# Kernel optimization log

Hardware: AMD Instinct MI355X
Metric: run time of the kernel (lower is better)

Reference implementation:

```python
import jax, jax.numpy as jnp
import numpy as np
import math

B, S, HID = 8, 512, 1024
H, D = 16, 64
SI = 64
MAXP = 512


def setup_inputs() -> dict:
    key = jax.random.key(0)
    ks = jax.random.split(key, 8)
    s = 1.0 / math.sqrt(HID)
    return {
        "hidden_states": jax.random.normal(ks[0], (B, S, HID), jnp.float32),
        "instruct_hidden_states": jax.random.normal(ks[1], (B, SI, HID), jnp.float32),
        "attention_mask": jnp.zeros((B, 1, 1, S), jnp.float32),
        "instruct_attention_mask": jnp.zeros((B, 1, 1, SI), jnp.float32),
        "Wq": jax.random.normal(ks[2], (HID, HID), jnp.float32) * s,
        "bq": jnp.zeros((HID,), jnp.float32),
        "Wk": jax.random.normal(ks[3], (HID, HID), jnp.float32) * s,
        "bk": jnp.zeros((HID,), jnp.float32),
        "Wv": jax.random.normal(ks[4], (HID, HID), jnp.float32) * s,
        "bv": jnp.zeros((HID,), jnp.float32),
        "dist_emb": jax.random.normal(ks[5], (2 * MAXP - 1, D), jnp.float32) * 0.02,
        "gate": jax.random.normal(ks[6], (1, H, 1, 1), jnp.float32) * 0.1,
    }


def _heads(x):
    # [B, L, H*D] -> [B, H, L, D]
    b, l, _ = x.shape
    return x.reshape(b, l, H, D).transpose(0, 2, 1, 3)


def reference(hidden_states, instruct_hidden_states, attention_mask,
              instruct_attention_mask, Wq, bq, Wk, bk, Wv, bv, dist_emb, gate):
    scale = 1.0 / math.sqrt(D)
    q = _heads(hidden_states @ Wq + bq)               # [B,H,S,D]
    k = _heads(hidden_states @ Wk + bk)
    v = _heads(hidden_states @ Wv + bv)
    ik = _heads(instruct_hidden_states @ Wk + bk)     # [B,H,Si,D]
    iv = _heads(instruct_hidden_states @ Wv + bv)

    # self-attention scores with relative_key_query position bias
    scores = jnp.einsum('bhld,bhrd->bhlr', q, k)
    pos = jnp.arange(S)
    dist = pos[:, None] - pos[None, :] + (MAXP - 1)   # [S,S] in [0, 2*MAXP-2]
    pe = dist_emb[dist]                                # [S,S,D]
    scores = scores + jnp.einsum('bhld,lrd->bhlr', q, pe) \
                    + jnp.einsum('bhrd,lrd->bhlr', k, pe)
    scores = scores * scale + attention_mask
    probs = jax.nn.softmax(scores, axis=-1)
    ctx = jnp.einsum('bhlr,bhrd->bhld', probs, v)

    # gated instruct attention branch
    iscores = jnp.einsum('bhld,bhrd->bhlr', q, ik) * scale + instruct_attention_mask
    iprobs = jax.nn.softmax(iscores, axis=-1)
    ictx = jnp.einsum('bhlr,bhrd->bhld', iprobs, iv)
    ctx = ctx + jnp.tanh(gate) * ictx

    return ctx.transpose(0, 2, 1, 3).reshape(B, S, HID)
```

## Files before the change

kernel.cpp:

```cpp
#include <hip/hip_runtime.h>

#define NH 16
#define DH 64
#define SEQ 512
#define SIN 64
#define NBATCH 8

#define L2E 1.4426950408889634f
#define C2  0.18033688011112043f
#define DEFER_THR 11.5412435f

typedef short bf16x8 __attribute__((ext_vector_type(8)));
typedef short bf16x4 __attribute__((ext_vector_type(4)));
typedef float f32x4 __attribute__((ext_vector_type(4)));

__device__ __forceinline__ unsigned short f2bf(float f) {
  union { float f; unsigned u; } v; v.f = f;
  unsigned r = v.u + 0x7FFFu + ((v.u >> 16) & 1u);
  return (unsigned short)(r >> 16);
}
__device__ __forceinline__ float bf2f(unsigned short b) {
  union { unsigned u; float f; } v; v.u = ((unsigned)b) << 16;
  return v.f;
}
__device__ __forceinline__ f32x4 mfma16(bf16x8 a, bf16x8 b, f32x4 c) {
  return __builtin_amdgcn_mfma_f32_16x16x32_bf16(a, b, c, 0, 0, 0);
}
__device__ __forceinline__ void gload_lds16(const unsigned short* g, unsigned short* l) {
  __builtin_amdgcn_global_load_lds((const __attribute__((address_space(1))) void*)g,
                                   (__attribute__((address_space(3))) void*)l, 16, 0, 0);
}

__device__ __forceinline__ void stage_tile_swz(const unsigned short* g, int gstride,
                                               unsigned short* lds, int w, int lane) {
  #pragma unroll
  for (int c = 0; c < 2; ++c) {
    const int row = w * 16 + c * 8 + (lane >> 3);
    const int cb = ((lane & 7) ^ (lane >> 3)) << 4;
    gload_lds16(g + (size_t)row * gstride + (cb >> 1),
                lds + (w * 16 + c * 8) * 64);
  }
}
__device__ __forceinline__ bf16x8 read_swz(const unsigned short* lds, int row, int colbyte) {
  return *(const bf16x8*)((const char*)(lds + row * 64) + (colbyte ^ ((row & 7) << 4)));
}

__global__ __launch_bounds__(256) void k_convert_all(const float* __restrict__ hs,
                                                     const float* __restrict__ ihs,
                                                     const float* __restrict__ de,
                                                     const float* __restrict__ Wq,
                                                     const float* __restrict__ Wk,
                                                     const float* __restrict__ Wv,
                                                     unsigned short* __restrict__ X,
                                                     unsigned short* __restrict__ E,
                                                     unsigned short* __restrict__ Wt) {
  __shared__ float t[64][65];
  const int bx = blockIdx.x, tid = threadIdx.x;
  if (bx < 4608) {
    int idx = bx * 256 + tid;
    float4 v;
    if (idx < 1048576) v = ((const float4*)hs)[idx];
    else               v = ((const float4*)ihs)[idx - 1048576];
    ushort4 o; o.x = f2bf(v.x); o.y = f2bf(v.y); o.z = f2bf(v.z); o.w = f2bf(v.w);
    ((ushort4*)X)[idx] = o;
  } else if (bx < 5376) {
    const int wb = bx - 4608;
    const int z = wb >> 8, rem = wb & 255;
    const float* W = (z == 0) ? Wq : (z == 1) ? Wk : Wv;
    const int n0 = (rem & 15) * 64, k0 = (rem >> 4) * 64;
    #pragma unroll
    for (int q = 0; q < 4; ++q) {
      int s = q * 256 + tid;
      int r = s >> 4, c4 = s & 15;
      float4 v = *(const float4*)(W + (size_t)(k0 + r) * 1024 + n0 + c4 * 4);
      t[r][c4 * 4 + 0] = v.x; t[r][c4 * 4 + 1] = v.y;
      t[r][c4 * 4 + 2] = v.z; t[r][c4 * 4 + 3] = v.w;
    }
    __syncthreads();
    #pragma unroll
    for (int q = 0; q < 4; ++q) {
      int s = q * 256 + tid;
      int rn = s >> 4, c4 = s & 15;
      ushort4 o;
      o.x = f2bf(t[c4 * 4 + 0][rn]); o.y = f2bf(t[c4 * 4 + 1][rn]);
      o.z = f2bf(t[c4 * 4 + 2][rn]); o.w = f2bf(t[c4 * 4 + 3][rn]);
      *(ushort4*)(Wt + ((size_t)(z << 10) + n0 + rn) * 1024 + k0 + c4 * 4) = o;
    }
  } else {
    int idx = (bx - 5376) * 256 + tid;
    ushort4 o;
    if (idx < 16368) {
      float4 v = ((const float4*)de)[idx];
      o.x = f2bf(v.x); o.y = f2bf(v.y); o.z = f2bf(v.z); o.w = f2bf(v.w);
    } else { o.x = 0; o.y = 0; o.z = 0; o.w = 0; }
    ((ushort4*)E)[idx] = o;
  }
}

__global__ __launch_bounds__(256) void k_gemm(const unsigned short* __restrict__ X,
                                              const unsigned short* __restrict__ Wt,
                                              const float* __restrict__ bq,
                                              const float* __restrict__ bk,
                                              const float* __restrict__ bv,
                                              unsigned short* __restrict__ Q,
                                              unsigned short* __restrict__ K,
                                              unsigned short* __restrict__ Vt,
                                              unsigned short* __restrict__ IK,
                                              unsigned short* __restrict__ IVt) {
  __shared__ unsigned short smem[16384];
  const int tid = threadIdx.x, lane = tid & 63, w = tid >> 6;
  const int lg = lane >> 4, lc = lane & 15;
  const int m0 = blockIdx.y * 128, n0 = blockIdx.x * 128;
  const int wm = (w >> 1) * 64, wn = (w & 1) * 64;
  const int which = n0 >> 10;
  const int h0 = (n0 & 1023) >> 6;
  const float* barr = (which == 0) ? bq : (which == 1) ? bk : bv;

  f32x4 acc[4][4];
  #pragma unroll
  for (int i = 0; i < 4; ++i)
    #pragma unroll
    for (int j = 0; j < 4; ++j) acc[i][j] = (f32x4){0.f, 0.f, 0.f, 0.f};

  const int ca = w * 128 + lane, cb2 = ca + 64;
  const unsigned short* ap0 = X  + (size_t)(m0 + (ca  >> 2)) * 1024 + (ca  & 3) * 8;
  const unsigned short* ap1 = X  + (size_t)(m0 + (cb2 >> 2)) * 1024 + (cb2 & 3) * 8;
  const unsigned short* bp0 = Wt + (size_t)(n0 + (ca  >> 2)) * 1024 + (ca  & 3) * 8;
  const unsigned short* bp1 = Wt + (size_t)(n0 + (cb2 >> 2)) * 1024 + (cb2 & 3) * 8;

  #define STAGE(bi)                                                   \
    {                                                                 \
      gload_lds16(ap0, smem + (bi) * 4096 + (w * 128) * 8);           \
      gload_lds16(ap1, smem + (bi) * 4096 + (w * 128 + 64) * 8);      \
      gload_lds16(bp0, smem + 8192 + (bi) * 4096 + (w * 128) * 8);    \
      gload_lds16(bp1, smem + 8192 + (bi) * 4096 + (w * 128 + 64) * 8); \
      ap0 += 32; ap1 += 32; bp0 += 32; bp1 += 32;                     \
    }

  STAGE(0);
  int cur = 0;
  for (int kt = 0; kt < 32; ++kt) {
    __syncthreads();
    if (kt + 1 < 32) STAGE(cur ^ 1);
    const unsigned short* A = smem + cur * 4096;
    const unsigned short* B = smem + 8192 + cur * 4096;
    bf16x8 af[4], bfr[4];
    #pragma unroll
    for (int i = 0; i < 4; ++i)
      af[i] = *(const bf16x8*)(A + (wm + i * 16 + lc) * 32 + lg * 8);
    #pragma unroll
    for (int j = 0; j < 4; ++j)
      bfr[j] = *(const bf16x8*)(B + (wn + j * 16 + lc) * 32 + lg * 8);
    #pragma unroll
    for (int i = 0; i < 4; ++i)
      #pragma unroll
      for (int j = 0; j < 4; ++j)
        acc[i][j] = mfma16(af[i], bfr[j], acc[i][j]);
    cur ^= 1;
  }
  #undef STAGE

  __syncthreads();
  {
    char* Cs = (char*)smem;
    #pragma unroll
    for (int j = 0; j < 4; ++j) {
      const float bias = barr[(n0 & 1023) + wn + j * 16 + lc];
      #pragma unroll
      for (int i = 0; i < 4; ++i)
        #pragma unroll
        for (int ii = 0; ii < 4; ++ii) {
          int row = wm + i * 16 + lg * 4 + ii;
          int col = wn + j * 16 + lc;
          if (which == 2) { int t = row; row = col; col = t; }
          *(unsigned short*)(Cs + row * 256 + ((col * 2) ^ ((row & 7) << 4))) =
              f2bf(acc[i][j][ii] + bias);
        }
    }
  }
  __syncthreads();
  {
    const char* Cs = (const char*)smem;
    const int row = tid >> 1, half = tid & 1;
    uint4 cvec[8];
    #pragma unroll
    for (int c8 = 0; c8 < 8; ++c8) {
      const int colb = half * 128 + c8 * 16;
      cvec[c8] = *(const uint4*)(Cs + row * 256 + (colb ^ ((row & 7) << 4)));
    }
    unsigned short* dst = nullptr;
    if (which != 2) {
      const int gm = m0 + row, hh = h0 + half;
      if (gm < 4096) {
        const int bb = gm >> 9, ss = gm & 511;
        unsigned short* base = (which == 0) ? Q : K;
        dst = base + (((size_t)(bb * NH + hh) * 512 + ss) << 6);
      } else if (which == 1) {
        const int mi = gm - 4096, bb = mi >> 6, si = mi & 63;
        dst = IK + (((size_t)(bb * NH + hh) * 64 + si) << 6);
      }
    } else {
      const int dd = row, hh = h0 + (dd >> 6), ddl = dd & 63;
      if (m0 < 4096) {
        const int bb = m0 >> 9, ss0 = (m0 & 511) + half * 64;
        dst = Vt + ((size_t)(bb * NH + hh) * 64 + ddl) * 512 + ss0;
      } else {
        const int mi0 = m0 - 4096 + half * 64, bb = mi0 >> 6;
        dst = IVt + (((size_t)(bb * NH + hh) * 64 + ddl) << 6);
      }
    }
    if (dst) {
      #pragma unroll
      for (int c8 = 0; c8 < 8; ++c8)
        *(uint4*)(dst + c8 * 8) = cvec[c8];
    }
  }
}

__global__ __launch_bounds__(256) void k_bias(const unsigned short* __restrict__ Qg,
                                              const unsigned short* __restrict__ Kg,
                                              const unsigned short* __restrict__ Eg,
                                              const float* __restrict__ mask,
                                              unsigned short* __restrict__ Bias) {
  const int rt = blockIdx.x, lt = blockIdx.y, bh = blockIdx.z;
  const int l0 = lt * 64, r0 = rt * 64;
  const int p0 = l0 - r0 + 448;
  const int tid = threadIdx.x, lane = tid & 63, w = tid >> 6;
  const int lg = lane >> 4, lc = lane & 15;
  const int ubase = w * 32;
  const int b = bh >> 4;

  __shared__ unsigned short Qs[64 * 64], Ks[64 * 64];
  __shared__ unsigned short qdl[64 * 128], kdl[64 * 128];

  stage_tile_swz(Qg + ((size_t)(bh * 512 + l0)) * 64, 64, Qs, w, lane);
  stage_tile_swz(Kg + ((size_t)(bh * 512 + r0)) * 64, 64, Ks, w, lane);

  bf16x8 eb[2][2];
  #pragma unroll
  for (int ns = 0; ns < 2; ++ns) {
    const int u = ubase + ns * 16 + lc;
    const unsigned short* ep = Eg + (size_t)(p0 + u) * 64 + lg * 8;
    eb[ns][0] = *(const bf16x8*)(ep);
    eb[ns][1] = *(const bf16x8*)(ep + 32);
  }
  __syncthreads();

  const int qswz = lg << 4;
  {
    f32x4 da[4][2];
    #pragma unroll
    for (int ms = 0; ms < 4; ++ms) { da[ms][0] = (f32x4){0,0,0,0}; da[ms][1] = (f32x4){0,0,0,0}; }
    #pragma unroll
    for (int kc = 0; kc < 2; ++kc)
      #pragma unroll
      for (int ms = 0; ms < 4; ++ms) {
        bf16x8 a = read_swz(Qs, ms * 16 + lc, kc * 64 + lg * 16);
        da[ms][0] = mfma16(a, eb[0][kc], da[ms][0]);
        da[ms][1] = mfma16(a, eb[1][kc], da[ms][1]);
      }
    #pragma unroll
    for (int ms = 0; ms < 4; ++ms)
      #pragma unroll
      for (int ns = 0; ns < 2; ++ns) {
        const int pc = (ubase + ns * 16 + lc) ^ qswz;
        #pragma unroll
        for (int i = 0; i < 4; ++i)
          qdl[(ms * 16 + lg * 4 + i) * 128 + pc] = f2bf(da[ms][ns][i]);
      }
    #pragma unroll
    for (int ms = 0; ms < 4; ++ms) { da[ms][0] = (f32x4){0,0,0,0}; da[ms][1] = (f32x4){0,0,0,0}; }
    #pragma unroll
    for (int kc = 0; kc < 2; ++kc)
      #pragma unroll
      for (int ms = 0; ms < 4; ++ms) {
        bf16x8 a = read_swz(Ks, ms * 16 + lc, kc * 64 + lg * 16);
        da[ms][0] = mfma16(a, eb[0][kc], da[ms][0]);
        da[ms][1] = mfma16(a, eb[1][kc], da[ms][1]);
      }
    #pragma unroll
    for (int ms = 0; ms < 4; ++ms)
      #pragma unroll
      for (int ns = 0; ns < 2; ++ns) {
        const int pc = (ubase + ns * 16 + lc) ^ qswz;
        #pragma unroll
        for (int i = 0; i < 4; ++i)
          kdl[(ms * 16 + lg * 4 + i) * 128 + pc] = f2bf(da[ms][ns][i]);
      }
  }
  __syncthreads();

  {
    unsigned short* dst = Bias + (((size_t)(bh * 64 + lt * 8 + rt)) << 12);
    const int rswz = (lc >> 2) << 4;
    #pragma unroll
    for (int ns = 0; ns < 4; ++ns) {
      const int ri = ns * 16 + lc;
      const float mk2 = mask[b * SEQ + r0 + ri] * L2E;
      ushort4 o;
      #pragma unroll
      for (int i = 0; i < 4; ++i) {
        const int li = w * 16 + lg * 4 + i;
        const int uq = li - ri + 63;
        const float qv = bf2f(qdl[li * 128 + (uq ^ qswz)]);
        const float kv = bf2f(kdl[ri * 128 + (uq ^ rswz)]);
        const unsigned short val = f2bf((qv + kv) * C2 + mk2);
        if (i == 0) o.x = val; else if (i == 1) o.y = val;
        else if (i == 2) o.z = val; else o.w = val;
      }
      *(ushort4*)(dst + (w * 4 + ns) * 256 + lane * 4) = o;
    }
  }
}

__global__ __launch_bounds__(256) void k_attn(const unsigned short* __restrict__ Qg,
                                              const unsigned short* __restrict__ Kg,
                                              const unsigned short* __restrict__ Vtg,
                                              const unsigned short* __restrict__ IKg,
                                              const unsigned short* __restrict__ IVtg,
                                              const unsigned short* __restrict__ Bias,
                                              const float* __restrict__ imask,
                                              const float* __restrict__ gate,
                                              float* __restrict__ out) {
  const int lt = blockIdx.x, h = blockIdx.y, b = blockIdx.z;
  const int l0 = lt * 64;
  const int tid = threadIdx.x;
  const int lane = tid & 63, w = tid >> 6;
  const int lg = lane >> 4, lc = lane & 15;
  const int bh = b * NH + h;

  __shared__ unsigned short Ks[2 * 64 * 64];
  __shared__ unsigned short Vts[2 * 64 * 64];
  __shared__ unsigned short Ps[64 * 64];

  bf16x8 qa[2];
  {
    const unsigned short* qrow = Qg + ((size_t)(bh * 512 + l0 + w * 16 + lc)) * 64;
    qa[0] = *(const bf16x8*)(qrow + lg * 8);
    qa[1] = *(const bf16x8*)(qrow + 32 + lg * 8);
  }

  f32x4 oacc[4];
  #pragma unroll
  for (int i = 0; i < 4; ++i) oacc[i] = (f32x4){0.f, 0.f, 0.f, 0.f};
  float mrun[4], lrun[4];
  #pragma unroll
  for (int i = 0; i < 4; ++i) { mrun[i] = -3.0e38f; lrun[i] = 0.f; }

  stage_tile_swz(Kg + ((size_t)(bh * 512)) * 64, 64, Ks, w, lane);
  stage_tile_swz(Vtg + (size_t)bh * 64 * 512, 512, Vts, w, lane);
  const unsigned short* btbase = Bias + (((size_t)(bh * 64 + lt * 8)) << 12);
  bf16x4 brow[4];
  #pragma unroll
  for (int ns = 0; ns < 4; ++ns)
    brow[ns] = *(const bf16x4*)(btbase + (w * 4 + ns) * 256 + lane * 4);

  for (int rt = 0; rt < 8; ++rt) {
    const int r0 = rt * 64;
    const int cur = rt & 1;
    __syncthreads();

    if (rt < 7) {
      stage_tile_swz(Kg + ((size_t)(bh * 512 + r0 + 64)) * 64, 64, Ks + (cur ^ 1) * 4096, w, lane);
      stage_tile_swz(Vtg + (size_t)bh * 64 * 512 + r0 + 64, 512, Vts + (cur ^ 1) * 4096, w, lane);
    } else {
      stage_tile_swz(IKg + (size_t)bh * 4096, 64, Ks, w, lane);
      stage_tile_swz(IVtg + (size_t)bh * 4096, 64, Vts, w, lane);
    }
    bf16x4 bnext[4];
    if (rt < 7) {
      const unsigned short* bt = btbase + ((size_t)(rt + 1) << 12);
      #pragma unroll
      for (int ns = 0; ns < 4; ++ns)
        bnext[ns] = *(const bf16x4*)(bt + (w * 4 + ns) * 256 + lane * 4);
    }

    const unsigned short* Kc = Ks + cur * 4096;
    const unsigned short* Vc = Vts + cur * 4096;

    f32x4 sacc[4];
    #pragma unroll
    for (int ns = 0; ns < 4; ++ns) sacc[ns] = (f32x4){0.f, 0.f, 0.f, 0.f};
    #pragma unroll
    for (int kc = 0; kc < 2; ++kc)
      #pragma unroll
      for (int ns = 0; ns < 4; ++ns) {
        bf16x8 kb = read_swz(Kc, ns * 16 + lc, kc * 64 + lg * 16);
        sacc[ns] = mfma16(qa[kc], kb, sacc[ns]);
      }
    float sv[4][4];
    #pragma unroll
    for (int ns = 0; ns < 4; ++ns)
      #pragma unroll
      for (int i = 0; i < 4; ++i)
        sv[ns][i] = fmaf(sacc[ns][i], C2, bf2f((unsigned short)brow[ns][i]));

    float mt[4];
    #pragma unroll
    for (int i = 0; i < 4; ++i) {
      float m_ = fmaxf(fmaxf(sv[0][i], sv[1][i]), fmaxf(sv[2][i], sv[3][i]));
      #pragma unroll
      for (int m = 1; m <= 8; m <<= 1) m_ = fmaxf(m_, __shfl_xor(m_, m));
      mt[i] = m_;
    }
    bool need = false;
    #pragma unroll
    for (int i = 0; i < 4; ++i) need = need || (mt[i] > mrun[i] + DEFER_THR);
    if (__any(need)) {
      #pragma unroll
      for (int i = 0; i < 4; ++i) {
        const float mnew = fmaxf(mrun[i], mt[i]);
        const float fr = exp2f(mrun[i] - mnew);
        mrun[i] = mnew;
        lrun[i] *= fr;
        #pragma unroll
        for (int ds = 0; ds < 4; ++ds) oacc[ds][i] *= fr;
      }
    }
    #pragma unroll
    for (int i = 0; i < 4; ++i) {
      float ps = 0.f;
      #pragma unroll
      for (int ns = 0; ns < 4; ++ns) { float p = exp2f(sv[ns][i] - mrun[i]); sv[ns][i] = p; ps += p; }
      #pragma unroll
      for (int m = 1; m <= 8; m <<= 1) ps += __shfl_xor(ps, m);
      lrun[i] += ps;
    }
    #pragma unroll
    for (int ns = 0; ns < 4; ++ns)
      #pragma unroll
      for (int i = 0; i < 4; ++i) {
        const int row = w * 16 + lg * 4 + i;
        const int cb = (ns * 16 + lc) * 2;
        *(unsigned short*)((char*)Ps + row * 128 + (cb ^ ((row & 7) << 4))) = f2bf(sv[ns][i]);
      }
    #pragma unroll
    for (int kc = 0; kc < 2; ++kc) {
      bf16x8 pa = read_swz(Ps, w * 16 + lc, kc * 64 + lg * 16);
      #pragma unroll
      for (int ds = 0; ds < 4; ++ds) {
        bf16x8 vb = read_swz(Vc, ds * 16 + lc, kc * 64 + lg * 16);
        oacc[ds] = mfma16(pa, vb, oacc[ds]);
      }
    }
    if (rt < 7) {
      #pragma unroll
      for (int ns = 0; ns < 4; ++ns) brow[ns] = bnext[ns];
    }
  }

  {
    __syncthreads();
    f32x4 sacc[4];
    #pragma unroll
    for (int ns = 0; ns < 4; ++ns) sacc[ns] = (f32x4){0.f, 0.f, 0.f, 0.f};
    #pragma unroll
    for (int kc = 0; kc < 2; ++kc)
      #pragma unroll
      for (int ns = 0; ns < 4; ++ns) {
        bf16x8 kb = read_swz(Ks, ns * 16 + lc, kc * 64 + lg * 16);
        sacc[ns] = mfma16(qa[kc], kb, sacc[ns]);
      }
    float sv[4][4], isum[4];
    #pragma unroll
    for (int ns = 0; ns < 4; ++ns) {
      const float mk2 = imask[b * SIN + ns * 16 + lc] * L2E;
      #pragma unroll
      for (int i = 0; i < 4; ++i) sv[ns][i] = fmaf(sacc[ns][i], C2, mk2);
    }
    #pragma unroll
    for (int i = 0; i < 4; ++i) {
      float mt = fmaxf(fmaxf(sv[0][i], sv[1][i]), fmaxf(sv[2][i], sv[3][i]));
      #pragma unroll
      for (int m = 1; m <= 8; m <<= 1) mt = fmaxf(mt, __shfl_xor(mt, m));
      float ps = 0.f;
      #pragma unroll
      for (int ns = 0; ns < 4; ++ns) { float p = exp2f(sv[ns][i] - mt); sv[ns][i] = p; ps += p; }
      #pragma unroll
      for (int m = 1; m <= 8; m <<= 1) ps += __shfl_xor(ps, m);
      isum[i] = ps;
    }
    #pragma unroll
    for (int ns = 0; ns < 4; ++ns)
      #pragma unroll
      for (int i = 0; i < 4; ++i) {
        const int row = w * 16 + lg * 4 + i;
        const int cb = (ns * 16 + lc) * 2;
        *(unsigned short*)((char*)Ps + row * 128 + (cb ^ ((row & 7) << 4))) = f2bf(sv[ns][i]);
      }
    f32x4 iacc[4];
    #pragma unroll
    for (int ds = 0; ds < 4; ++ds) iacc[ds] = (f32x4){0.f, 0.f, 0.f, 0.f};
    #pragma unroll
    for (int kc = 0; kc < 2; ++kc) {
      bf16x8 pa = read_swz(Ps, w * 16 + lc, kc * 64 + lg * 16);
      #pragma unroll
      for (int ds = 0; ds < 4; ++ds) {
        bf16x8 vb = read_swz(Vts, ds * 16 + lc, kc * 64 + lg * 16);
        iacc[ds] = mfma16(pa, vb, iacc[ds]);
      }
    }
    const float tg = tanhf(gate[h]);
    #pragma unroll
    for (int ds = 0; ds < 4; ++ds)
      #pragma unroll
      for (int i = 0; i < 4; ++i) {
        const int li = w * 16 + lg * 4 + i;
        const float val = oacc[ds][i] / lrun[i] + tg * (iacc[ds][i] / isum[i]);
        out[(size_t)(b * SEQ + l0 + li) * 1024 + h * 64 + ds * 16 + lc] = val;
      }
  }
}


extern "C" void kernel_launch(void* const* d_in, const int* in_sizes, int n_in,
                              void* d_out, int out_size, void* d_ws, size_t ws_size,
                              hipStream_t stream) {
  (void)in_sizes; (void)n_in; (void)out_size; (void)ws_size;
  const float* hs    = (const float*)d_in[0];
  const float* ihs   = (const float*)d_in[1];
  const float* mask  = (const float*)d_in[2];
  const float* imask = (const float*)d_in[3];
  const float* Wq    = (const float*)d_in[4];
  const float* bq    = (const float*)d_in[5];
  const float* Wk    = (const float*)d_in[6];
  const float* bk    = (const float*)d_in[7];
  const float* Wv    = (const float*)d_in[8];
  const float* bv    = (const float*)d_in[9];
  const float* de    = (const float*)d_in[10];
  const float* gate  = (const float*)d_in[11];
  float* out = (float*)d_out;

  char* ws = (char*)d_ws;
  size_t off = 0;
  auto alloc = [&](size_t bytes) -> void* {
    void* p = ws + off;
    off += (bytes + 255) & ~(size_t)255;
    return p;
  };
  unsigned short* X    = (unsigned short*)alloc((size_t)4608 * 1024 * 2);
  unsigned short* Wt   = (unsigned short*)alloc((size_t)3072 * 1024 * 2);
  unsigned short* E    = (unsigned short*)alloc((size_t)1024 * 64 * 2);
  unsigned short* Qb   = (unsigned short*)alloc((size_t)8 * 16 * 512 * 64 * 2);
  unsigned short* Kb   = (unsigned short*)alloc((size_t)8 * 16 * 512 * 64 * 2);
  unsigned short* Vtb  = (unsigned short*)alloc((size_t)8 * 16 * 64 * 512 * 2);
  unsigned short* IKb  = (unsigned short*)alloc((size_t)8 * 16 * 64 * 64 * 2);
  unsigned short* IVtb = (unsigned short*)alloc((size_t)8 * 16 * 64 * 64 * 2);
  unsigned short* Bias = (unsigned short*)alloc((size_t)128 * 64 * 4096 * 2);

  k_convert_all<<<5440, 256, 0, stream>>>(hs, ihs, de, Wq, Wk, Wv, X, E, Wt);
  k_gemm<<<dim3(24, 36), 256, 0, stream>>>(X, Wt, bq, bk, bv, Qb, Kb, Vtb, IKb, IVtb);
  k_bias<<<dim3(8, 8, 128), 256, 0, stream>>>(Qb, Kb, E, mask, Bias);
  k_attn<<<dim3(8, 16, 8), 256, 0, stream>>>(Qb, Kb, Vtb, IKb, IVtb, Bias, imask, gate, out);
}
```

Baseline: 159.6 us.

## Enlarge QKV projection GEMM tile to 256x256 with 512 threads

The fused QKV GEMM moves from 128x128 tiles with 4 waves to 256x256 tiles with 8 waves, each wave computing 128x64. The aim is more operand reuse per LDS load and fewer blocks re-reading X and Wt from global memory. The epilogue now writes the output in two rounds with a wider LDS swizzle. In exchange the grid drops from 864 to 216 blocks, which is fewer than the GPU has CUs, and the kernel uses 128KB of LDS plus more registers per thread, so occupancy and load balance may suffer.

```diff
diff --git a/kernel.cpp b/kernel.cpp
--- a/kernel.cpp
+++ b/kernel.cpp
@@ -97,7 +97,7 @@
   }
 }
 
-__global__ __launch_bounds__(256) void k_gemm(const unsigned short* __restrict__ X,
+__global__ __launch_bounds__(512) void k_gemm(const unsigned short* __restrict__ X,
                                               const unsigned short* __restrict__ Wt,
                                               const float* __restrict__ bq,
                                               const float* __restrict__ bk,
@@ -107,34 +107,34 @@
                                               unsigned short* __restrict__ Vt,
                                               unsigned short* __restrict__ IK,
                                               unsigned short* __restrict__ IVt) {
-  __shared__ unsigned short smem[16384];
+  __shared__ unsigned short smem[65536];
   const int tid = threadIdx.x, lane = tid & 63, w = tid >> 6;
   const int lg = lane >> 4, lc = lane & 15;
-  const int m0 = blockIdx.y * 128, n0 = blockIdx.x * 128;
-  const int wm = (w >> 1) * 64, wn = (w & 1) * 64;
+  const int m0 = blockIdx.y * 256, n0 = blockIdx.x * 256;
+  const int wr = w >> 2, wc = w & 3;
   const int which = n0 >> 10;
   const int h0 = (n0 & 1023) >> 6;
   const float* barr = (which == 0) ? bq : (which == 1) ? bk : bv;
 
-  f32x4 acc[4][4];
+  f32x4 acc[8][4];
   #pragma unroll
-  for (int i = 0; i < 4; ++i)
+  for (int i = 0; i < 8; ++i)
     #pragma unroll
     for (int j = 0; j < 4; ++j) acc[i][j] = (f32x4){0.f, 0.f, 0.f, 0.f};
 
-  const int ca = w * 128 + lane, cb2 = ca + 64;
-  const unsigned short* ap0 = X  + (size_t)(m0 + (ca  >> 2)) * 1024 + (ca  & 3) * 8;
-  const unsigned short* ap1 = X  + (size_t)(m0 + (cb2 >> 2)) * 1024 + (cb2 & 3) * 8;
-  const unsigned short* bp0 = Wt + (size_t)(n0 + (ca  >> 2)) * 1024 + (ca  & 3) * 8;
-  const unsigned short* bp1 = Wt + (size_t)(n0 + (cb2 >> 2)) * 1024 + (cb2 & 3) * 8;
-
-  #define STAGE(bi)                                                   \
-    {                                                                 \
-      gload_lds16(ap0, smem + (bi) * 4096 + (w * 128) * 8);           \
-      gload_lds16(ap1, smem + (bi) * 4096 + (w * 128 + 64) * 8);      \
-      gload_lds16(bp0, smem + 8192 + (bi) * 4096 + (w * 128) * 8);    \
-      gload_lds16(bp1, smem + 8192 + (bi) * 4096 + (w * 128 + 64) * 8); \
-      ap0 += 32; ap1 += 32; bp0 += 32; bp1 += 32;                     \
+  const int c0 = w * 128 + lane, c1 = c0 + 64;
+  const unsigned short* ap0 = X  + (size_t)(m0 + (c0 >> 2)) * 1024 + (c0 & 3) * 8;
+  const unsigned short* ap1 = X  + (size_t)(m0 + (c1 >> 2)) * 1024 + (c1 & 3) * 8;
+  const unsigned short* bp0 = Wt + (size_t)(n0 + (c0 >> 2)) * 1024 + (c0 & 3) * 8;
+  const unsigned short* bp1 = Wt + (size_t)(n0 + (c1 >> 2)) * 1024 + (c1 & 3) * 8;
+
+  #define STAGE(bi)                                                       \
+    {                                                                     \
+      gload_lds16(ap0, smem + (bi) * 8192 + (w * 128) * 8);               \
+      gload_lds16(ap1, smem + (bi) * 8192 + (w * 128 + 64) * 8);          \
+      gload_lds16(bp0, smem + 16384 + (bi) * 8192 + (w * 128) * 8);       \
+      gload_lds16(bp1, smem + 16384 + (bi) * 8192 + (w * 128 + 64) * 8);  \
+      ap0 += 32; ap1 += 32; bp0 += 32; bp1 += 32;                         \
     }
 
   STAGE(0);
@@ -142,17 +142,17 @@
   for (int kt = 0; kt < 32; ++kt) {
     __syncthreads();
     if (kt + 1 < 32) STAGE(cur ^ 1);
-    const unsigned short* A = smem + cur * 4096;
-    const unsigned short* B = smem + 8192 + cur * 4096;
-    bf16x8 af[4], bfr[4];
-    #pragma unroll
-    for (int i = 0; i < 4; ++i)
-      af[i] = *(const bf16x8*)(A + (wm + i * 16 + lc) * 32 + lg * 8);
+    const unsigned short* A = smem + cur * 8192;
+    const unsigned short* B = smem + 16384 + cur * 8192;
+    bf16x8 af[8], bfr[4];
+    #pragma unroll
+    for (int i = 0; i < 8; ++i)
+      af[i] = *(const bf16x8*)(A + (wr * 128 + i * 16 + lc) * 32 + lg * 8);
     #pragma unroll
     for (int j = 0; j < 4; ++j)
-      bfr[j] = *(const bf16x8*)(B + (wn + j * 16 + lc) * 32 + lg * 8);
-    #pragma unroll
-    for (int i = 0; i < 4; ++i)
+      bfr[j] = *(const bf16x8*)(B + (wc * 64 + j * 16 + lc) * 32 + lg * 8);
+    #pragma unroll
+    for (int i = 0; i < 8; ++i)
       #pragma unroll
       for (int j = 0; j < 4; ++j)
         acc[i][j] = mfma16(af[i], bfr[j], acc[i][j]);
@@ -165,15 +165,15 @@
     char* Cs = (char*)smem;
     #pragma unroll
     for (int j = 0; j < 4; ++j) {
-      const float bias = barr[(n0 & 1023) + wn + j * 16 + lc];
-      #pragma unroll
-      for (int i = 0; i < 4; ++i)
+      const float bias = barr[(n0 & 1023) + wc * 64 + j * 16 + lc];
+      #pragma unroll
+      for (int i = 0; i < 8; ++i)
         #pragma unroll
         for (int ii = 0; ii < 4; ++ii) {
-          int row = wm + i * 16 + lg * 4 + ii;
-          int col = wn + j * 16 + lc;
+          int row = wr * 128 + i * 16 + lg * 4 + ii;
+          int col = wc * 64 + j * 16 + lc;
           if (which == 2) { int t = row; row = col; col = t; }
-          *(unsigned short*)(Cs + row * 256 + ((col * 2) ^ ((row & 7) << 4))) =
+          *(unsigned short*)(Cs + row * 512 + ((col * 2) ^ (((row >> 2) & 31) << 4))) =
               f2bf(acc[i][j][ii] + bias);
         }
     }
@@ -181,38 +181,42 @@
   __syncthreads();
   {
     const char* Cs = (const char*)smem;
-    const int row = tid >> 1, half = tid & 1;
-    uint4 cvec[8];
-    #pragma unroll
-    for (int c8 = 0; c8 < 8; ++c8) {
-      const int colb = half * 128 + c8 * 16;
-      cvec[c8] = *(const uint4*)(Cs + row * 256 + (colb ^ ((row & 7) << 4)));
-    }
-    unsigned short* dst = nullptr;
-    if (which != 2) {
-      const int gm = m0 + row, hh = h0 + half;
-      if (gm < 4096) {
-        const int bb = gm >> 9, ss = gm & 511;
-        unsigned short* base = (which == 0) ? Q : K;
-        dst = base + (((size_t)(bb * NH + hh) * 512 + ss) << 6);
-      } else if (which == 1) {
-        const int mi = gm - 4096, bb = mi >> 6, si = mi & 63;
-        dst = IK + (((size_t)(bb * NH + hh) * 64 + si) << 6);
-      }
-    } else {
-      const int dd = row, hh = h0 + (dd >> 6), ddl = dd & 63;
-      if (m0 < 4096) {
-        const int bb = m0 >> 9, ss0 = (m0 & 511) + half * 64;
-        dst = Vt + ((size_t)(bb * NH + hh) * 64 + ddl) * 512 + ss0;
+    const int row = tid >> 1;
+    #pragma unroll
+    for (int rnd = 0; rnd < 2; ++rnd) {
+      const int q = (tid & 1) + rnd * 2;
+      uint4 cvec[8];
+      #pragma unroll
+      for (int c8 = 0; c8 < 8; ++c8)
+        cvec[c8] = *(const uint4*)(Cs + row * 512 +
+                                   ((q * 128 + c8 * 16) ^ (((row >> 2) & 31) << 4)));
+      unsigned short* dst = nullptr;
+      if (which != 2) {
+        const int gm = m0 + row, hh = h0 + q;
+        if (gm < 4096) {
+          const int bb = gm >> 9, ss = gm & 511;
+          unsigned short* base = (which == 0) ? Q : K;
+          dst = base + (((size_t)(bb * NH + hh) * 512 + ss) << 6);
+        } else if (which == 1) {
+          const int mi = gm - 4096, bb = mi >> 6, si = mi & 63;
+          dst = IK + (((size_t)(bb * NH + hh) * 64 + si) << 6);
+        }
       } else {
-        const int mi0 = m0 - 4096 + half * 64, bb = mi0 >> 6;
-        dst = IVt + (((size_t)(bb * NH + hh) * 64 + ddl) << 6);
-      }
-    }
-    if (dst) {
-      #pragma unroll
-      for (int c8 = 0; c8 < 8; ++c8)
-        *(uint4*)(dst + c8 * 8) = cvec[c8];
+        const int dd = row, hh = h0 + (dd >> 6), ddl = dd & 63;
+        const int gm0 = m0 + q * 64;
+        if (gm0 < 4096) {
+          const int bb = gm0 >> 9, ss0 = gm0 & 511;
+          dst = Vt + ((size_t)(bb * NH + hh) * 64 + ddl) * 512 + ss0;
+        } else {
+          const int mi0 = gm0 - 4096, bb = mi0 >> 6;
+          dst = IVt + (((size_t)(bb * NH + hh) * 64 + ddl) << 6);
+        }
+      }
+      if (dst) {
+        #pragma unroll
+        for (int c8 = 0; c8 < 8; ++c8)
+          *(uint4*)(dst + c8 * 8) = cvec[c8];
+      }
     }
   }
 }
@@ -549,7 +553,7 @@
   unsigned short* Bias = (unsigned short*)alloc((size_t)128 * 64 * 4096 * 2);
 
   k_convert_all<<<5440, 256, 0, stream>>>(hs, ihs, de, Wq, Wk, Wv, X, E, Wt);
-  k_gemm<<<dim3(24, 36), 256, 0, stream>>>(X, Wt, bq, bk, bv, Qb, Kb, Vtb, IKb, IVtb);
+  k_gemm<<<dim3(12, 18), 512, 0, stream>>>(X, Wt, bq, bk, bv, Qb, Kb, Vtb, IKb, IVtb);
   k_bias<<<dim3(8, 8, 128), 256, 0, stream>>>(Qb, Kb, E, mask, Bias);
   k_attn<<<dim3(8, 16, 8), 256, 0, stream>>>(Qb, Kb, Vtb, IKb, IVtb, Bias, imask, gate, out);
 }
```

New measurement: 152.2 us. 1.05x faster.
